# Performance work log

Measured on AMD Instinct MI355X. Metric: run time of the kernel, lower is better.

Reference implementation:

```python
import jax, jax.numpy as jnp
import numpy as np

N, E = 50000, 800000
D_IN, HID, H, C, E_DIM = 128, 128, 4, 32, 32  # C = HID // H


def setup_inputs() -> dict:
    key = jax.random.key(0)
    ks = jax.random.split(key, 16)
    def lin(k, fan_in, fan_out):
        return jax.random.normal(k, (fan_in, fan_out), jnp.float32) / np.sqrt(fan_in)
    return {
        "x": jax.random.normal(ks[0], (N, D_IN), jnp.float32),
        "edge_index": jax.random.randint(ks[1], (2, E), 0, N, jnp.int32),
        "edge_attr": jax.random.normal(ks[2], (E, E_DIM), jnp.float32),
        # TransformerConv params (bias=True on q/k/v and skip; lin_edge has no bias in PyG)
        "Wq": lin(ks[3], D_IN, HID), "bq": jnp.zeros((HID,), jnp.float32),
        "Wk": lin(ks[4], D_IN, HID), "bk": jnp.zeros((HID,), jnp.float32),
        "Wv": lin(ks[5], D_IN, HID), "bv": jnp.zeros((HID,), jnp.float32),
        "We": lin(ks[6], E_DIM, HID),
        "Wskip": lin(ks[7], D_IN, HID), "bskip": jnp.zeros((HID,), jnp.float32),
        # MLP([HID, HID, HID]) -> two Linear layers, GELU(tanh) after each (plain_last=False)
        "W1": lin(ks[8], HID, HID), "b1": jnp.zeros((HID,), jnp.float32),
        "W2": lin(ks[9], HID, HID), "b2": jnp.zeros((HID,), jnp.float32),
    }


def reference(x, edge_index, edge_attr, Wq, bq, Wk, bk, Wv, bv, We, Wskip, bskip, W1, b1, W2, b2):
    src, dst = edge_index[0], edge_index[1]  # messages flow src(j) -> dst(i)
    n = x.shape[0]
    q = (x @ Wq + bq).reshape(n, H, C)
    k = (x @ Wk + bk).reshape(n, H, C)
    v = (x @ Wv + bv).reshape(n, H, C)
    e = (edge_attr @ We).reshape(-1, H, C)          # [E,H,C]
    kj = k[src] + e                                  # gather + edge lift
    vj = v[src] + e
    alpha = jnp.einsum("ehc,ehc->eh", q[dst], kj) / np.sqrt(C)  # [E,H]
    # segment softmax over destination neighborhoods (PyG softmax semantics)
    amax = jax.ops.segment_max(alpha, dst, num_segments=n)      # [N,H]
    amax = jnp.where(jnp.isfinite(amax), amax, 0.0)
    ex = jnp.exp(alpha - amax[dst])
    denom = jax.ops.segment_sum(ex, dst, num_segments=n)
    alpha = ex / (denom[dst] + 1e-16)
    # (attention dropout p=0.3 is inactive in eval mode)
    agg = jax.ops.segment_sum(vj * alpha[:, :, None], dst, num_segments=n)  # [N,H,C]
    out = agg.reshape(n, HID) + (x @ Wskip + bskip)  # concat heads + root skip
    # residual MLP: gelu(tanh) after every layer since plain_last=False, norm=None
    h = jax.nn.gelu(out @ W1 + b1, approximate=True)
    h = jax.nn.gelu(h @ W2 + b2, approximate=True)
    return out + h
```

## Files before the change

kernel.cpp:

```cpp
#include <hip/hip_runtime.h>
#include <math.h>


#define D 128
#define EDIM 32

using bf16x8 = __attribute__((ext_vector_type(8))) short;
using f32x4  = __attribute__((ext_vector_type(4))) float;
using ushort8 = __attribute__((ext_vector_type(8))) unsigned short;

__device__ inline unsigned short f2bf(float f) {
    unsigned int u = __float_as_uint(f);
    u += 0x7FFFu + ((u >> 16) & 1u);
    return (unsigned short)(u >> 16);
}
__device__ inline float bf2f(unsigned short h) {
    return __uint_as_float(((unsigned int)h) << 16);
}
__device__ inline float gelu_fast(float x) {
    float x3 = x * x * x;
    float u = 0.7978845608028654f * (x + 0.044715f * x3);
    float t = 1.f - 2.f / (__expf(2.f * u) + 1.f);
    return 0.5f * x * (1.f + t);
}
__device__ inline float quad_add(float x) {
    int a = __builtin_amdgcn_update_dpp(0, __float_as_int(x), 0xB1, 0xF, 0xF, true);
    x += __int_as_float(a);
    a = __builtin_amdgcn_update_dpp(0, __float_as_int(x), 0x4E, 0xF, 0xF, true);
    x += __int_as_float(a);
    return x;
}

__device__ inline bf16x8 ldsB(const unsigned short* sw, int col, int kk0) {
    return *(const bf16x8*)(sw + col * 128 + (kk0 ^ ((col & 7) << 3)));
}

__global__ __launch_bounds__(128) void prep_bqe(
    const float* __restrict__ bq, const float* __restrict__ We,
    float* __restrict__ bqE)
{
    const int j = threadIdx.x;
    const int hb = j & 96, k = j & 31;
    const float* wek = We + (size_t)k * D + hb;
    float s = 0.f;
#pragma unroll 8
    for (int c = 0; c < 32; ++c) s = fmaf(bq[hb + c], wek[c], s);
    bqE[j] = s;
}

__global__ __launch_bounds__(256) void prep_wt(
    const float* __restrict__ Wq, const float* __restrict__ Wk,
    const float* __restrict__ Wv, const float* __restrict__ Wsk,
    const float* __restrict__ W1, const float* __restrict__ W2,
    const float* __restrict__ We, unsigned short* __restrict__ Wt)
{
    int t = blockIdx.x * 256 + threadIdx.x;
    int m = t >> 14;
    int r = t & 16383;
    int col = r & 127, kk = r >> 7;
    float v;
    if (m < 6) {
        const float* W = (m == 0) ? Wq : (m == 1) ? Wk : (m == 2) ? Wv
                       : (m == 3) ? Wsk : (m == 4) ? W1 : W2;
        v = W[(size_t)kk * D + col];
    } else if (m == 6) {
        const int hb = col & 96;
        const float* wqr = Wq + (size_t)kk * D + hb;
        const float* wer = We + (size_t)(col & 31) * D + hb;
        float s = 0.f;
#pragma unroll 8
        for (int c = 0; c < 32; ++c) s = fmaf(wqr[c], wer[c], s);
        v = s;
    } else {
        v = ((kk >> 5) == (col >> 5)) ? We[(size_t)(kk & 31) * D + col] : 0.f;
    }
    Wt[(size_t)m * 16384 + (size_t)col * 128 + (kk ^ ((col & 7) << 3))] = f2bf(v);
}

__global__ __launch_bounds__(256) void gemm_qkvs(
    const float* __restrict__ x, const unsigned short* __restrict__ Wt,
    const float* __restrict__ bq, const float* __restrict__ bk,
    const float* __restrict__ bv, const float* __restrict__ bs,
    const float* __restrict__ bqE,
    unsigned short* __restrict__ Q, unsigned short* __restrict__ K,
    unsigned short* __restrict__ V, float* __restrict__ S,
    float* __restrict__ QE, int N)
{
    __shared__ unsigned short sw[16384];
    const int m = blockIdx.y;
    const int widx = (m < 4) ? m : 6;
    const int t = threadIdx.x;
    const int lane = t & 63;
    const int w = t >> 6;
    const int row0 = blockIdx.x * 64 + w * 16;
    const int lrow = lane & 15;
    const int kb = (lane >> 4) * 8;
    const int rq = (lane >> 4) * 4;

    const unsigned short* gsrc = Wt + (size_t)widx * 16384;
    ushort8 stg[8];
#pragma unroll
    for (int it = 0; it < 8; ++it)
        stg[it] = *(const ushort8*)(gsrc + (t + it * 256) * 8);

    bf16x8 af[4];
    {
        int ar = row0 + lrow; if (ar > N - 1) ar = N - 1;
        const float* xr = x + (size_t)ar * D + kb;
#pragma unroll
        for (int kf = 0; kf < 4; ++kf) {
            float4 p0 = *(const float4*)(xr + kf * 32);
            float4 p1 = *(const float4*)(xr + kf * 32 + 4);
            bf16x8 a;
            a[0] = (short)f2bf(p0.x); a[1] = (short)f2bf(p0.y);
            a[2] = (short)f2bf(p0.z); a[3] = (short)f2bf(p0.w);
            a[4] = (short)f2bf(p1.x); a[5] = (short)f2bf(p1.y);
            a[6] = (short)f2bf(p1.z); a[7] = (short)f2bf(p1.w);
            af[kf] = a;
        }
    }

#pragma unroll
    for (int it = 0; it < 8; ++it)
        *(ushort8*)(&sw[(t + it * 256) * 8]) = stg[it];
    __syncthreads();

    const float* bias = (m == 0) ? bq : (m == 1) ? bk : (m == 2) ? bv
                      : (m == 3) ? bs : bqE;
    f32x4 acc[8];
#pragma unroll
    for (int nf = 0; nf < 8; ++nf) acc[nf] = (f32x4){0.f, 0.f, 0.f, 0.f};
#pragma unroll
    for (int nf = 0; nf < 8; ++nf) {
        const int col = nf * 16 + lrow;
#pragma unroll
        for (int kf = 0; kf < 4; ++kf)
            acc[nf] = __builtin_amdgcn_mfma_f32_16x16x32_bf16(
                af[kf], ldsB(sw, col, kf * 32 + kb), acc[nf], 0, 0, 0);
    }
#pragma unroll
    for (int nf = 0; nf < 8; ++nf) {
        const int col = nf * 16 + lrow;
        const float bb = bias[col];
#pragma unroll
        for (int i = 0; i < 4; ++i) {
            int r = row0 + rq + i;
            if (r < N) {
                float v = acc[nf][i] + bb;
                size_t o = (size_t)r * D + col;
                if (m == 0) Q[o] = f2bf(v);
                else if (m == 1) K[o] = f2bf(v);
                else if (m == 2) V[o] = f2bf(v);
                else if (m == 3) S[o] = v;
                else QE[o] = v;
            }
        }
    }
}

__global__ __launch_bounds__(256) void hist_kernel(
    const int* __restrict__ EI, int* __restrict__ deg, int E)
{
    int e = blockIdx.x * 256 + threadIdx.x;
    if (e < E) atomicAdd(&deg[EI[E + e]], 1);
}

__global__ __launch_bounds__(1024) void scanA(
    const int* __restrict__ deg, int* __restrict__ rowptr,
    int* __restrict__ psums, int N)
{
    __shared__ int tmp[1024];
    const int t = threadIdx.x;
    const int i = blockIdx.x * 1024 + t;
    int v = (i < N) ? deg[i] : 0;
    tmp[t] = v;
    __syncthreads();
    for (int off = 1; off < 1024; off <<= 1) {
        int add = (t >= off) ? tmp[t - off] : 0;
        __syncthreads();
        tmp[t] += add;
        __syncthreads();
    }
    if (i < N) rowptr[i + 1] = tmp[t];
    if (t == 1023) psums[blockIdx.x] = tmp[1023];
}

__global__ __launch_bounds__(1024) void scanB(int* __restrict__ psums, int nb)
{
    __shared__ int tmp[1024];
    const int t = threadIdx.x;
    int v = (t < nb) ? psums[t] : 0;
    tmp[t] = v;
    __syncthreads();
    for (int off = 1; off < 1024; off <<= 1) {
        int add = (t >= off) ? tmp[t - off] : 0;
        __syncthreads();
        tmp[t] += add;
        __syncthreads();
    }
    if (t < nb) psums[t] = tmp[t] - v;
}

__global__ __launch_bounds__(256) void scanC(
    int* __restrict__ rowptr, int* __restrict__ cursor,
    const int* __restrict__ psums, int N)
{
    int i = blockIdx.x * 256 + threadIdx.x;
    if (i == 0) { rowptr[0] = 0; cursor[0] = 0; }
    if (i < N) {
        int val = rowptr[i + 1] + psums[i >> 10];
        rowptr[i + 1] = val;
        if (i + 1 < N) cursor[i + 1] = val;
    }
}

__global__ __launch_bounds__(256) void scatter_kernel(
    const int* __restrict__ EI, const float* __restrict__ EA,
    int* __restrict__ cursor, int* __restrict__ srcs,
    unsigned short* __restrict__ EAP, int E)
{
    int e = blockIdx.x * 256 + threadIdx.x;
    if (e >= E) return;
    int dst = EI[E + e];
    int pos = atomicAdd(&cursor[dst], 1);
    srcs[pos] = EI[e];
    const float4* s4 = (const float4*)(EA + (size_t)e * EDIM);
    unsigned short* op = EAP + (size_t)pos * EDIM;
#pragma unroll
    for (int j = 0; j < 4; ++j) {
        float4 a = s4[2 * j], b = s4[2 * j + 1];
        ushort8 u;
        u[0] = f2bf(a.x); u[1] = f2bf(a.y); u[2] = f2bf(a.z); u[3] = f2bf(a.w);
        u[4] = f2bf(b.x); u[5] = f2bf(b.y); u[6] = f2bf(b.z); u[7] = f2bf(b.w);
        *(ushort8*)(op + j * 8) = u;
    }
}

__global__ __launch_bounds__(256) void gather_pass(
    const int* __restrict__ rowptr, const int* __restrict__ srcs,
    const unsigned short* __restrict__ EAP,
    const unsigned short* __restrict__ Q, const unsigned short* __restrict__ K,
    const unsigned short* __restrict__ V, const float* __restrict__ QE,
    float* __restrict__ SB, unsigned short* __restrict__ SAS, int N)
{
    const int lane = threadIdx.x & 63;
    const int wid = threadIdx.x >> 6;
    const int n = blockIdx.x * 4 + wid;
    if (n >= N) return;
    const int g = lane & 15;
    const int grp = lane >> 4;

    float q8[8], qe8[8];
    {
        bf16x8 qb = *(const bf16x8*)(Q + (size_t)n * D + g * 8);
#pragma unroll
        for (int j = 0; j < 8; ++j) q8[j] = bf2f((unsigned short)qb[j]);
        float4 a = *(const float4*)(QE + (size_t)n * D + g * 8);
        float4 b = *(const float4*)(QE + (size_t)n * D + g * 8 + 4);
        qe8[0] = a.x; qe8[1] = a.y; qe8[2] = a.z; qe8[3] = a.w;
        qe8[4] = b.x; qe8[5] = b.y; qe8[6] = b.z; qe8[7] = b.w;
    }

    float acc[8], sa[8], den = 0.f;
#pragma unroll
    for (int j = 0; j < 8; ++j) { acc[j] = 0.f; sa[j] = 0.f; }

    const int i0 = rowptr[n], i1 = rowptr[n + 1];

    int idx = i0 + grp;
    int src_c = (idx < i1) ? srcs[idx] : -1;

    for (int base = i0; base < i1; base += 4, idx += 4) {
        const int src = src_c;
        {
            int idx_n = idx + 4;
            src_c = (idx_n < i1) ? srcs[idx_n] : -1;
        }
        bf16x8 kb = {0,0,0,0,0,0,0,0};
        bf16x8 vb = {0,0,0,0,0,0,0,0};
        bf16x8 eb = {0,0,0,0,0,0,0,0};
        if (src >= 0) {
            kb = *(const bf16x8*)(K + (size_t)src * D + g * 8);
            vb = *(const bf16x8*)(V + (size_t)src * D + g * 8);
            eb = *(const bf16x8*)(EAP + (size_t)idx * EDIM + (g & 3) * 8);
        }
        float ef[8], vf[8];
        float p = 0.f;
#pragma unroll
        for (int j = 0; j < 8; ++j) {
            float kf = bf2f((unsigned short)kb[j]);
            ef[j] = bf2f((unsigned short)eb[j]);
            vf[j] = bf2f((unsigned short)vb[j]);
            p = fmaf(q8[j], kf, fmaf(ef[j], qe8[j], p));
        }
        p = quad_add(p);
        float ex = (src >= 0) ? __expf(p * 0.17677669529663689f) : 0.f;
        den += ex;
#pragma unroll
        for (int j = 0; j < 8; ++j) {
            acc[j] = fmaf(ex, vf[j], acc[j]);
            sa[j]  = fmaf(ex, ef[j], sa[j]);
        }
    }

#pragma unroll
    for (int off = 16; off <= 32; off <<= 1) {
        den += __shfl_xor(den, off, 64);
#pragma unroll
        for (int j = 0; j < 8; ++j) {
            acc[j] += __shfl_xor(acc[j], off, 64);
            sa[j]  += __shfl_xor(sa[j],  off, 64);
        }
    }

    if (grp == 0) {
        const float rden = 1.f / (den + 1e-16f);
        float* so = SB + (size_t)n * D + g * 8;
        unsigned short* po = SAS + (size_t)n * D + g * 8;
#pragma unroll
        for (int j = 0; j < 8; ++j) {
            so[j] = fmaf(acc[j], rden, so[j]);
            po[j] = f2bf(sa[j] * rden);
        }
    }
}

__global__ __launch_bounds__(256) void combine_mlp1(
    float* __restrict__ SB, const unsigned short* __restrict__ SAS,
    const unsigned short* __restrict__ WtC, const unsigned short* __restrict__ Wt1,
    const float* __restrict__ b1, unsigned short* __restrict__ H1, int N)
{
    __shared__ unsigned short sw[16384];
    __shared__ unsigned short bounce[64 * 136];
    const int t = threadIdx.x;
    const int lane = t & 63;
    const int w = t >> 6;
    const int row0 = blockIdx.x * 64 + w * 16;
    const int lrow = lane & 15;
    const int kb = (lane >> 4) * 8;
    const int rq = (lane >> 4) * 4;

    ushort8 stg[8];
#pragma unroll
    for (int it = 0; it < 8; ++it)
        stg[it] = *(const ushort8*)(WtC + (t + it * 256) * 8);

    bf16x8 af[4];
    {
        int ar = row0 + lrow; if (ar > N - 1) ar = N - 1;
        const unsigned short* xr = SAS + (size_t)ar * D + kb;
#pragma unroll
        for (int kf = 0; kf < 4; ++kf) af[kf] = *(const bf16x8*)(xr + kf * 32);
    }
    f32x4 acc[8];
#pragma unroll
    for (int nf = 0; nf < 8; ++nf) {
        const int col = nf * 16 + lrow;
#pragma unroll
        for (int i = 0; i < 4; ++i) {
            int r = row0 + rq + i;
            acc[nf][i] = (r < N) ? SB[(size_t)r * D + col] : 0.f;
        }
    }

#pragma unroll
    for (int it = 0; it < 8; ++it)
        *(ushort8*)(&sw[(t + it * 256) * 8]) = stg[it];
    __syncthreads();

#pragma unroll
    for (int nf = 0; nf < 8; ++nf) {
        const int col = nf * 16 + lrow;
#pragma unroll
        for (int kf = 0; kf < 4; ++kf)
            acc[nf] = __builtin_amdgcn_mfma_f32_16x16x32_bf16(
                af[kf], ldsB(sw, col, kf * 32 + kb), acc[nf], 0, 0, 0);
    }
    __syncthreads();

#pragma unroll
    for (int it = 0; it < 8; ++it)
        stg[it] = *(const ushort8*)(Wt1 + (t + it * 256) * 8);
#pragma unroll
    for (int nf = 0; nf < 8; ++nf) {
        const int col = nf * 16 + lrow;
#pragma unroll
        for (int i = 0; i < 4; ++i) {
            int r = row0 + rq + i;
            float v = acc[nf][i];
            bounce[(w * 16 + rq + i) * 136 + col] = f2bf(v);
            if (r < N) SB[(size_t)r * D + col] = v;
        }
    }
#pragma unroll
    for (int it = 0; it < 8; ++it)
        *(ushort8*)(&sw[(t + it * 256) * 8]) = stg[it];
    __syncthreads();

    bf16x8 af2[4];
#pragma unroll
    for (int kf = 0; kf < 4; ++kf)
        af2[kf] = *(const bf16x8*)(&bounce[(w * 16 + lrow) * 136 + kb + kf * 32]);
    f32x4 acc2[8];
#pragma unroll
    for (int nf = 0; nf < 8; ++nf) acc2[nf] = (f32x4){0.f, 0.f, 0.f, 0.f};
#pragma unroll
    for (int nf = 0; nf < 8; ++nf) {
        const int col = nf * 16 + lrow;
#pragma unroll
        for (int kf = 0; kf < 4; ++kf)
            acc2[nf] = __builtin_amdgcn_mfma_f32_16x16x32_bf16(
                af2[kf], ldsB(sw, col, kf * 32 + kb), acc2[nf], 0, 0, 0);
    }
#pragma unroll
    for (int nf = 0; nf < 8; ++nf) {
        const int col = nf * 16 + lrow;
        const float bb = b1[col];
#pragma unroll
        for (int i = 0; i < 4; ++i) {
            int r = row0 + rq + i;
            if (r < N) H1[(size_t)r * D + col] = f2bf(gelu_fast(acc2[nf][i] + bb));
        }
    }
}

__global__ __launch_bounds__(256) void mlp2_kernel(
    const unsigned short* __restrict__ H1, const float* __restrict__ OUT,
    const unsigned short* __restrict__ Wt2, const float* __restrict__ b2,
    float* __restrict__ FINAL, int N)
{
    __shared__ unsigned short sw[16384];
    const int t = threadIdx.x;
    const int lane = t & 63;
    const int w = t >> 6;
    const int row0 = blockIdx.x * 64 + w * 16;
    const int lrow = lane & 15;
    const int kb = (lane >> 4) * 8;
    const int rq = (lane >> 4) * 4;

    ushort8 stg[8];
#pragma unroll
    for (int it = 0; it < 8; ++it)
        stg[it] = *(const ushort8*)(Wt2 + (t + it * 256) * 8);

    bf16x8 af[4];
    {
        int ar = row0 + lrow; if (ar > N - 1) ar = N - 1;
        const unsigned short* xr = H1 + (size_t)ar * D + kb;
#pragma unroll
        for (int kf = 0; kf < 4; ++kf) af[kf] = *(const bf16x8*)(xr + kf * 32);
    }

#pragma unroll
    for (int it = 0; it < 8; ++it)
        *(ushort8*)(&sw[(t + it * 256) * 8]) = stg[it];
    __syncthreads();

    f32x4 acc[8];
#pragma unroll
    for (int nf = 0; nf < 8; ++nf) acc[nf] = (f32x4){0.f, 0.f, 0.f, 0.f};
#pragma unroll
    for (int nf = 0; nf < 8; ++nf) {
        const int col = nf * 16 + lrow;
#pragma unroll
        for (int kf = 0; kf < 4; ++kf)
            acc[nf] = __builtin_amdgcn_mfma_f32_16x16x32_bf16(
                af[kf], ldsB(sw, col, kf * 32 + kb), acc[nf], 0, 0, 0);
    }
#pragma unroll
    for (int nf = 0; nf < 8; ++nf) {
        const int col = nf * 16 + lrow;
        const float bb = b2[col];
#pragma unroll
        for (int i = 0; i < 4; ++i) {
            int r = row0 + rq + i;
            if (r < N) {
                size_t o = (size_t)r * D + col;
                FINAL[o] = OUT[o] + gelu_fast(acc[nf][i] + bb);
            }
        }
    }
}

extern "C" void kernel_launch(void* const* d_in, const int* in_sizes, int n_in,
                              void* d_out, int out_size, void* d_ws, size_t ws_size,
                              hipStream_t stream)
{
    const float* x   = (const float*)d_in[0];
    const int*   EI  = (const int*)  d_in[1];
    const float* EA  = (const float*)d_in[2];
    const float* Wq  = (const float*)d_in[3];
    const float* bq  = (const float*)d_in[4];
    const float* Wk  = (const float*)d_in[5];
    const float* bk  = (const float*)d_in[6];
    const float* Wv  = (const float*)d_in[7];
    const float* bv  = (const float*)d_in[8];
    const float* We  = (const float*)d_in[9];
    const float* Wsk = (const float*)d_in[10];
    const float* bsk = (const float*)d_in[11];
    const float* W1  = (const float*)d_in[12];
    const float* b1  = (const float*)d_in[13];
    const float* W2  = (const float*)d_in[14];
    const float* b2  = (const float*)d_in[15];

    const int N = in_sizes[0] / D;
    const int E = in_sizes[1] / 2;

    char* p = (char*)d_ws;
    auto alloc = [&](size_t bytes) -> void* {
        void* r = (void*)p;
        p += (bytes + 255) & ~(size_t)255;
        return r;
    };
    float*          Sb     = (float*)         alloc((size_t)N * D * 4);
    float*          QEb    = (float*)         alloc((size_t)N * D * 4);
    unsigned short* Qb     = (unsigned short*)alloc((size_t)N * D * 2);
    unsigned short* Kb     = (unsigned short*)alloc((size_t)N * D * 2);
    unsigned short* Vb     = (unsigned short*)alloc((size_t)N * D * 2);
    unsigned short* SASb   = (unsigned short*)alloc((size_t)N * D * 2);
    unsigned short* EAPb   = (unsigned short*)alloc((size_t)E * EDIM * 2);
    int*            srcsb  = (int*)           alloc((size_t)E * 4);
    unsigned short* Wt     = (unsigned short*)alloc((size_t)8 * 16384 * 2);
    float*          bqEb   = (float*)         alloc((size_t)128 * 4);
    int*            deg    = (int*)           alloc((size_t)N * 4);
    int*            rowptr = (int*)           alloc((size_t)(N + 1) * 4);
    int*            cursor = (int*)           alloc((size_t)(N + 1) * 4);
    int*            psums  = (int*)           alloc((size_t)1024 * 4);

    unsigned short* H1b = (unsigned short*)QEb;

    hipMemsetAsync(deg, 0, (size_t)N * sizeof(int), stream);

    const int NB = (N + 63) / 64;
    const int EB = (E + 255) / 256;
    const int SB_ = (N + 1023) / 1024;

    prep_bqe<<<1, 128, 0, stream>>>(bq, We, bqEb);
    prep_wt<<<(8 * 16384) / 256, 256, 0, stream>>>(Wq, Wk, Wv, Wsk, W1, W2,
                                                   We, Wt);

    gemm_qkvs<<<dim3(NB, 5), 256, 0, stream>>>(x, Wt, bq, bk, bv, bsk, bqEb,
                                               Qb, Kb, Vb, Sb, QEb, N);

    hist_kernel<<<EB, 256, 0, stream>>>(EI, deg, E);
    scanA<<<SB_, 1024, 0, stream>>>(deg, rowptr, psums, N);
    scanB<<<1, 1024, 0, stream>>>(psums, SB_);
    scanC<<<(N + 255) / 256, 256, 0, stream>>>(rowptr, cursor, psums, N);
    scatter_kernel<<<EB, 256, 0, stream>>>(EI, EA, cursor, srcsb, EAPb, E);

    gather_pass<<<(N + 3) / 4, 256, 0, stream>>>(
        rowptr, srcsb, EAPb, Qb, Kb, Vb, QEb, Sb, SASb, N);

    combine_mlp1<<<NB, 256, 0, stream>>>(Sb, SASb, Wt + (size_t)7 * 16384,
                                         Wt + (size_t)4 * 16384, b1, H1b, N);
    mlp2_kernel<<<NB, 256, 0, stream>>>(H1b, Sb, Wt + (size_t)5 * 16384, b2,
                                        (float*)d_out, N);
}
```

Baseline: 305.8 us.

## Interleave K/V and Q/QE in bf16, unroll gather by two edges, fuse prep kernels

Packs K and V into one interleaved row and stores Q alongside a bf16 version of QE (previously fp32), so each gathered neighbour's K and V come from one 512-byte row. The gather loop now processes two edges per group per iteration with srcs prefetched one step ahead, which gives more loads in flight. The bqE prep kernel is folded into prep_wt to save a launch. QE in bf16 costs some precision, and the two-edge loop adds register pressure.

Result: faster. 299.2 us (-2.2%).

```diff
diff --git a/kernel.cpp b/kernel.cpp
--- a/kernel.cpp
+++ b/kernel.cpp
@@ -35,28 +35,27 @@
     return *(const bf16x8*)(sw + col * 128 + (kk0 ^ ((col & 7) << 3)));
 }
 
-__global__ __launch_bounds__(128) void prep_bqe(
-    const float* __restrict__ bq, const float* __restrict__ We,
-    float* __restrict__ bqE)
-{
-    const int j = threadIdx.x;
-    const int hb = j & 96, k = j & 31;
-    const float* wek = We + (size_t)k * D + hb;
-    float s = 0.f;
-#pragma unroll 8
-    for (int c = 0; c < 32; ++c) s = fmaf(bq[hb + c], wek[c], s);
-    bqE[j] = s;
-}
-
 __global__ __launch_bounds__(256) void prep_wt(
     const float* __restrict__ Wq, const float* __restrict__ Wk,
     const float* __restrict__ Wv, const float* __restrict__ Wsk,
     const float* __restrict__ W1, const float* __restrict__ W2,
-    const float* __restrict__ We, unsigned short* __restrict__ Wt)
+    const float* __restrict__ We, const float* __restrict__ bq,
+    unsigned short* __restrict__ Wt, float* __restrict__ bqE)
 {
     int t = blockIdx.x * 256 + threadIdx.x;
     int m = t >> 14;
     int r = t & 16383;
+    if (m >= 8) {
+        if (r < 128) {
+            const int hb = r & 96, k = r & 31;
+            const float* wek = We + (size_t)k * D + hb;
+            float s = 0.f;
+#pragma unroll 8
+            for (int c = 0; c < 32; ++c) s = fmaf(bq[hb + c], wek[c], s);
+            bqE[r] = s;
+        }
+        return;
+    }
     int col = r & 127, kk = r >> 7;
     float v;
     if (m < 6) {
@@ -82,9 +81,8 @@
     const float* __restrict__ bq, const float* __restrict__ bk,
     const float* __restrict__ bv, const float* __restrict__ bs,
     const float* __restrict__ bqE,
-    unsigned short* __restrict__ Q, unsigned short* __restrict__ K,
-    unsigned short* __restrict__ V, float* __restrict__ S,
-    float* __restrict__ QE, int N)
+    unsigned short* __restrict__ QA, unsigned short* __restrict__ KV,
+    float* __restrict__ S, int N)
 {
     __shared__ unsigned short sw[16384];
     const int m = blockIdx.y;
@@ -147,12 +145,11 @@
             int r = row0 + rq + i;
             if (r < N) {
                 float v = acc[nf][i] + bb;
-                size_t o = (size_t)r * D + col;
-                if (m == 0) Q[o] = f2bf(v);
-                else if (m == 1) K[o] = f2bf(v);
-                else if (m == 2) V[o] = f2bf(v);
-                else if (m == 3) S[o] = v;
-                else QE[o] = v;
+                if (m == 0)      QA[(size_t)r * 256 + col]       = f2bf(v);
+                else if (m == 1) KV[(size_t)r * 256 + col]       = f2bf(v);
+                else if (m == 2) KV[(size_t)r * 256 + 128 + col] = f2bf(v);
+                else if (m == 3) S[(size_t)r * D + col]          = v;
+                else             QA[(size_t)r * 256 + 128 + col] = f2bf(v);
             }
         }
     }
@@ -239,8 +236,7 @@
 __global__ __launch_bounds__(256) void gather_pass(
     const int* __restrict__ rowptr, const int* __restrict__ srcs,
     const unsigned short* __restrict__ EAP,
-    const unsigned short* __restrict__ Q, const unsigned short* __restrict__ K,
-    const unsigned short* __restrict__ V, const float* __restrict__ QE,
+    const unsigned short* __restrict__ QA, const unsigned short* __restrict__ KV,
     float* __restrict__ SB, unsigned short* __restrict__ SAS, int N)
 {
     const int lane = threadIdx.x & 63;
@@ -249,16 +245,18 @@
     if (n >= N) return;
     const int g = lane & 15;
     const int grp = lane >> 4;
+    const int eoff = (g & 3) * 8;
 
     float q8[8], qe8[8];
     {
-        bf16x8 qb = *(const bf16x8*)(Q + (size_t)n * D + g * 8);
-#pragma unroll
-        for (int j = 0; j < 8; ++j) q8[j] = bf2f((unsigned short)qb[j]);
-        float4 a = *(const float4*)(QE + (size_t)n * D + g * 8);
-        float4 b = *(const float4*)(QE + (size_t)n * D + g * 8 + 4);
-        qe8[0] = a.x; qe8[1] = a.y; qe8[2] = a.z; qe8[3] = a.w;
-        qe8[4] = b.x; qe8[5] = b.y; qe8[6] = b.z; qe8[7] = b.w;
+        const unsigned short* qa = QA + (size_t)n * 256 + g * 8;
+        bf16x8 qb  = *(const bf16x8*)(qa);
+        bf16x8 qeb = *(const bf16x8*)(qa + 128);
+#pragma unroll
+        for (int j = 0; j < 8; ++j) {
+            q8[j]  = bf2f((unsigned short)qb[j]);
+            qe8[j] = bf2f((unsigned short)qeb[j]);
+        }
     }
 
     float acc[8], sa[8], den = 0.f;
@@ -267,40 +265,67 @@
 
     const int i0 = rowptr[n], i1 = rowptr[n + 1];
 
-    int idx = i0 + grp;
-    int src_c = (idx < i1) ? srcs[idx] : -1;
-
-    for (int base = i0; base < i1; base += 4, idx += 4) {
-        const int src = src_c;
+    int iA = i0 + grp, iB = iA + 4;
+    int sA = (iA < i1) ? srcs[iA] : -1;
+    int sB = (iB < i1) ? srcs[iB] : -1;
+
+    for (int b = i0; b < i1; b += 8) {
+        const int iA2 = iA + 8, iB2 = iB + 8;
+        const int sA2 = (iA2 < i1) ? srcs[iA2] : -1;
+        const int sB2 = (iB2 < i1) ? srcs[iB2] : -1;
+
+        bf16x8 kA = {0,0,0,0,0,0,0,0}, vA = kA, eA = kA;
+        bf16x8 kB = kA, vB = kA, eB = kA;
+        if (sA >= 0) {
+            const unsigned short* kv = KV + (size_t)sA * 256 + g * 8;
+            kA = *(const bf16x8*)(kv);
+            vA = *(const bf16x8*)(kv + 128);
+            eA = *(const bf16x8*)(EAP + (size_t)iA * EDIM + eoff);
+        }
+        if (sB >= 0) {
+            const unsigned short* kv = KV + (size_t)sB * 256 + g * 8;
+            kB = *(const bf16x8*)(kv);
+            vB = *(const bf16x8*)(kv + 128);
+            eB = *(const bf16x8*)(EAP + (size_t)iB * EDIM + eoff);
+        }
+
         {
-            int idx_n = idx + 4;
-            src_c = (idx_n < i1) ? srcs[idx_n] : -1;
-        }
-        bf16x8 kb = {0,0,0,0,0,0,0,0};
-        bf16x8 vb = {0,0,0,0,0,0,0,0};
-        bf16x8 eb = {0,0,0,0,0,0,0,0};
-        if (src >= 0) {
-            kb = *(const bf16x8*)(K + (size_t)src * D + g * 8);
-            vb = *(const bf16x8*)(V + (size_t)src * D + g * 8);
-            eb = *(const bf16x8*)(EAP + (size_t)idx * EDIM + (g & 3) * 8);
-        }
-        float ef[8], vf[8];
-        float p = 0.f;
-#pragma unroll
-        for (int j = 0; j < 8; ++j) {
-            float kf = bf2f((unsigned short)kb[j]);
-            ef[j] = bf2f((unsigned short)eb[j]);
-            vf[j] = bf2f((unsigned short)vb[j]);
-            p = fmaf(q8[j], kf, fmaf(ef[j], qe8[j], p));
-        }
-        p = quad_add(p);
-        float ex = (src >= 0) ? __expf(p * 0.17677669529663689f) : 0.f;
-        den += ex;
-#pragma unroll
-        for (int j = 0; j < 8; ++j) {
-            acc[j] = fmaf(ex, vf[j], acc[j]);
-            sa[j]  = fmaf(ex, ef[j], sa[j]);
-        }
+            float ef[8];
+            float p = 0.f;
+#pragma unroll
+            for (int j = 0; j < 8; ++j) {
+                ef[j] = bf2f((unsigned short)eA[j]);
+                p = fmaf(q8[j], bf2f((unsigned short)kA[j]),
+                         fmaf(ef[j], qe8[j], p));
+            }
+            p = quad_add(p);
+            const float ex = (sA >= 0) ? __expf(p * 0.17677669529663689f) : 0.f;
+            den += ex;
+#pragma unroll
+            for (int j = 0; j < 8; ++j) {
+                acc[j] = fmaf(ex, bf2f((unsigned short)vA[j]), acc[j]);
+                sa[j]  = fmaf(ex, ef[j], sa[j]);
+            }
+        }
+        {
+            float ef[8];
+            float p = 0.f;
+#pragma unroll
+            for (int j = 0; j < 8; ++j) {
+                ef[j] = bf2f((unsigned short)eB[j]);
+                p = fmaf(q8[j], bf2f((unsigned short)kB[j]),
+                         fmaf(ef[j], qe8[j], p));
+            }
+            p = quad_add(p);
+            const float ex = (sB >= 0) ? __expf(p * 0.17677669529663689f) : 0.f;
+            den += ex;
+#pragma unroll
+            for (int j = 0; j < 8; ++j) {
+                acc[j] = fmaf(ex, bf2f((unsigned short)vB[j]), acc[j]);
+                sa[j]  = fmaf(ex, ef[j], sa[j]);
+            }
+        }
+        iA = iA2; iB = iB2; sA = sA2; sB = sB2;
     }
 
 #pragma unroll
@@ -513,10 +538,8 @@
         return r;
     };
     float*          Sb     = (float*)         alloc((size_t)N * D * 4);
-    float*          QEb    = (float*)         alloc((size_t)N * D * 4);
-    unsigned short* Qb     = (unsigned short*)alloc((size_t)N * D * 2);
-    unsigned short* Kb     = (unsigned short*)alloc((size_t)N * D * 2);
-    unsigned short* Vb     = (unsigned short*)alloc((size_t)N * D * 2);
+    unsigned short* QAb    = (unsigned short*)alloc((size_t)N * 256 * 2);
+    unsigned short* KVb    = (unsigned short*)alloc((size_t)N * 256 * 2);
     unsigned short* SASb   = (unsigned short*)alloc((size_t)N * D * 2);
     unsigned short* EAPb   = (unsigned short*)alloc((size_t)E * EDIM * 2);
     int*            srcsb  = (int*)           alloc((size_t)E * 4);
@@ -527,7 +550,7 @@
     int*            cursor = (int*)           alloc((size_t)(N + 1) * 4);
     int*            psums  = (int*)           alloc((size_t)1024 * 4);
 
-    unsigned short* H1b = (unsigned short*)QEb;
+    unsigned short* H1b = QAb;
 
     hipMemsetAsync(deg, 0, (size_t)N * sizeof(int), stream);
 
@@ -535,12 +558,10 @@
     const int EB = (E + 255) / 256;
     const int SB_ = (N + 1023) / 1024;
 
-    prep_bqe<<<1, 128, 0, stream>>>(bq, We, bqEb);
-    prep_wt<<<(8 * 16384) / 256, 256, 0, stream>>>(Wq, Wk, Wv, Wsk, W1, W2,
-                                                   We, Wt);
+    prep_wt<<<513, 256, 0, stream>>>(Wq, Wk, Wv, Wsk, W1, W2, We, bq, Wt, bqEb);
 
     gemm_qkvs<<<dim3(NB, 5), 256, 0, stream>>>(x, Wt, bq, bk, bv, bsk, bqEb,
-                                               Qb, Kb, Vb, Sb, QEb, N);
+                                               QAb, KVb, Sb, N);
 
     hist_kernel<<<EB, 256, 0, stream>>>(EI, deg, E);
     scanA<<<SB_, 1024, 0, stream>>>(deg, rowptr, psums, N);
@@ -549,7 +570,7 @@
     scatter_kernel<<<EB, 256, 0, stream>>>(EI, EA, cursor, srcsb, EAPb, E);
 
     gather_pass<<<(N + 3) / 4, 256, 0, stream>>>(
-        rowptr, srcsb, EAPb, Qb, Kb, Vb, QEb, Sb, SASb, N);
+        rowptr, srcsb, EAPb, QAb, KVb, Sb, SASb, N);
 
     combine_mlp1<<<NB, 256, 0, stream>>>(Sb, SASb, Wt + (size_t)7 * 16384,
                                          Wt + (size_t)4 * 16384, b1, H1b, N);
```
